# Kernel tuning notes

Hardware: AMD Instinct MI355X
Metric: run time of the kernel (lower is better)

Reference implementation:

```python
import jax, jax.numpy as jnp
import numpy as np

B, T, D, N, K, H = 2, 2048, 3584, 16, 8, 256
WINDOW = 1024
SOFT_CAP = 50.0
SCALAR = 0.0625  # head_dim ** -0.5
BASE = 10000.0
K_MASK = -2.3819763e38


def apply_rope(x, pos):
    # x: [B, S, heads, H], pos: [B, S]
    frac = 2.0 * jnp.arange(H // 2, dtype=jnp.float32) / H
    timescale = BASE ** frac  # [H/2]
    sinusoid = pos[..., None].astype(jnp.float32) / timescale  # [B, S, H/2]
    sinusoid = sinusoid[..., None, :]  # [B, S, 1, H/2]
    sin, cos = jnp.sin(sinusoid), jnp.cos(sinusoid)
    first, second = jnp.split(x, 2, axis=-1)
    out = jnp.concatenate([first * cos - second * sin,
                           second * cos + first * sin], axis=-1)
    return out.astype(x.dtype)


def setup_inputs() -> dict:
    key = jax.random.key(0)
    ks = jax.random.split(key, 4)
    x = jax.random.normal(ks[0], (B, T, D), jnp.float32)
    q_w = jax.random.normal(ks[1], (N, D, H), jnp.float32) * 0.02
    kv_w = jax.random.normal(ks[2], (2, K, D, H), jnp.float32) * 0.02
    o_w = jax.random.normal(ks[3], (N, H, D), jnp.float32) * 0.02
    segment_pos = jnp.broadcast_to(jnp.arange(T, dtype=jnp.int32), (B, T))
    attn_mask = jnp.tril(jnp.ones((1, T, T), dtype=bool))  # causal [#B, T, S]
    return {"x": x, "segment_pos": segment_pos, "attn_mask": attn_mask,
            "q_w": q_w, "kv_w": kv_w, "o_w": o_w}


def reference(x, segment_pos, attn_mask, q_w, kv_w, o_w):
    # Projections (GQA path: num_kv_heads != num_heads)
    q = jnp.einsum('BTD,NDH->BTNH', x, q_w)
    kv = jnp.einsum('BSD,CKDH->CBSKH', x, kv_w)
    k, v = kv[0], kv[1]
    # RoPE on keys and queries, then query scaling
    k = apply_rope(k, segment_pos)
    q = apply_rope(q, segment_pos) * SCALAR
    # GQA: group N query heads over K kv heads
    G = N // K
    qg = q.reshape(B, T, K, G, H)
    logits = jnp.einsum('BTKGH,BSKH->BTKGS', qg, k).reshape(B, T, N, T)
    # Logit soft cap
    logits = jnp.tanh(logits / SOFT_CAP) * SOFT_CAP
    # Sliding-window causal mask (attn_mask is causal, S > window)
    mask = jnp.triu(attn_mask, 1 - WINDOW)  # [#B, T, S]
    padded = jnp.where(mask[:, :, None, :], logits, K_MASK)
    probs = jax.nn.softmax(padded, axis=-1).astype(k.dtype)
    enc = jnp.einsum('BTKGS,BSKH->BTKGH', probs.reshape(B, T, K, G, T), v)
    enc = enc.reshape(B, T, N, H)
    out = jnp.einsum('BTNH,NHD->BTD', enc, o_w)
    no_attended = jnp.all(mask == 0, axis=-1, keepdims=True)  # [#B, T, 1]
    return jnp.where(no_attended, jnp.zeros_like(out), out)
```

## Files before the change

kernel.cpp:

```cpp
#include <hip/hip_runtime.h>
#include <stdint.h>


typedef short bf16x8 __attribute__((ext_vector_type(8)));
typedef float f32x4 __attribute__((ext_vector_type(4)));

#define MFMA16(a, b, c) __builtin_amdgcn_mfma_f32_16x16x32_bf16((a), (b), (c), 0, 0, 0)

__device__ __forceinline__ uint16_t f2bf(float f) {
  uint32_t u = __builtin_bit_cast(uint32_t, f);
  u += 0x7FFFu + ((u >> 16) & 1u);
  return (uint16_t)(u >> 16);
}
__device__ __forceinline__ float bf2f(uint16_t u) {
  return __builtin_bit_cast(float, (uint32_t)u << 16);
}
__device__ __forceinline__ void async16(void* lds, const void* g) {
  __builtin_amdgcn_global_load_lds(
      (const __attribute__((address_space(1))) uint32_t*)g,
      (__attribute__((address_space(3))) uint32_t*)lds, 16, 0, 0);
}

__global__ void convert_x(const float* __restrict__ x, uint16_t* __restrict__ xb) {
  size_t i = ((size_t)blockIdx.x * 256 + threadIdx.x) * 8;
  f32x4 a = *(const f32x4*)(x + i);
  f32x4 b = *(const f32x4*)(x + i + 4);
  bf16x8 r;
  r[0] = (short)f2bf(a[0]); r[1] = (short)f2bf(a[1]);
  r[2] = (short)f2bf(a[2]); r[3] = (short)f2bf(a[3]);
  r[4] = (short)f2bf(b[0]); r[5] = (short)f2bf(b[1]);
  r[6] = (short)f2bf(b[2]); r[7] = (short)f2bf(b[3]);
  *(bf16x8*)(xb + i) = r;
}

__global__ void transpose_qkvw(const float* __restrict__ qw,
                               const float* __restrict__ kvw,
                               uint16_t* __restrict__ WqkvT) {
  __shared__ uint16_t tile[64][65];
  const int j0 = blockIdx.x * 64;
  const int d0 = blockIdx.y * 64;
  const int t = threadIdx.x;
  const int jl = t & 63;
  const int q4 = t >> 6;
  const int j = j0 + jl;
  const float* src;
  if (j0 < 4096) {
    src = qw + (size_t)(j >> 8) * 3584 * 256 + (j & 255);
  } else {
    int j2 = j - 4096;
    src = kvw + ((size_t)((j2 >> 11) * 8 + ((j2 >> 8) & 7)) * 3584) * 256 + (j2 & 255);
  }
#pragma unroll
  for (int r = 0; r < 16; ++r) {
    int dl = r * 4 + q4;
    tile[jl][dl] = f2bf(src[(size_t)(d0 + dl) * 256]);
  }
  __syncthreads();
#pragma unroll
  for (int r = 0; r < 16; ++r) {
    int jl2 = r * 4 + q4;
    WqkvT[(size_t)(j0 + jl2) * 3584 + d0 + jl] = tile[jl2][jl];
  }
}

__global__ void transpose_ow(const float* __restrict__ ow, uint16_t* __restrict__ WoT) {
  __shared__ uint16_t tile[64][65];
  const int d0 = blockIdx.x * 64;
  const int j0 = blockIdx.y * 64;
  const int t = threadIdx.x;
  const int c = t & 63;
  const int q4 = t >> 6;
#pragma unroll
  for (int r = 0; r < 16; ++r) {
    int jl = r * 4 + q4;
    tile[c][jl] = f2bf(ow[(size_t)(j0 + jl) * 3584 + d0 + c]);
  }
  __syncthreads();
#pragma unroll
  for (int r = 0; r < 16; ++r) {
    int dl = r * 4 + q4;
    WoT[(size_t)(d0 + dl) * 4096 + j0 + c] = tile[dl][c];
  }
}

template <int EPI>
__global__ __launch_bounds__(512, 2) void gemm256(
    const uint16_t* __restrict__ A, const uint16_t* __restrict__ Bt,
    int Kd, int Nc, int nbx,
    void* __restrict__ Oqv, uint16_t* __restrict__ Ok, uint16_t* __restrict__ Ov) {
  __shared__ uint16_t lds[4 * 16384];

  const int tid = threadIdx.x;
  const int lane = tid & 63;
  const int quad = lane >> 4;
  const int l15 = lane & 15;
  const int wave = tid >> 6;
  const int wm = wave & 1;
  const int wn = wave >> 1;

  const int nwg = gridDim.x;
  const int chunk = nwg >> 3;
  const int wg = blockIdx.x;
  const int swz = (wg & 7) * chunk + (wg >> 3);
  const int by = swz / nbx;
  const int bx = swz - by * nbx;
  const int m0 = by * 256;
  const int n0 = bx * 256;

  f32x4 acc[8][4];
#pragma unroll
  for (int i = 0; i < 8; ++i)
#pragma unroll
    for (int j = 0; j < 4; ++j) acc[i][j] = f32x4{0.f, 0.f, 0.f, 0.f};

  const int srow = tid >> 2;
  const int sck = tid & 3;
  const int gck0 = sck ^ ((srow >> 1) & 3);
  const int gck1 = sck ^ (((srow + 128) >> 1) & 3);
  const uint16_t* gA0 = A + (size_t)(m0 + srow) * Kd + gck0 * 8;
  const uint16_t* gA1 = A + (size_t)(m0 + srow + 128) * Kd + gck1 * 8;
  const uint16_t* gB0 = Bt + (size_t)(n0 + srow) * Kd + gck0 * 8;
  const uint16_t* gB1 = Bt + (size_t)(n0 + srow + 128) * Kd + gck1 * 8;

  const int T = Kd >> 5;

#pragma unroll
  for (int pt = 0; pt < 3; ++pt) {
    uint16_t* sd = lds + pt * 16384;
    const int kt = pt * 32;
    async16(sd + tid * 8, gA0 + kt);
    async16(sd + 4096 + tid * 8, gA1 + kt);
    async16(sd + 8192 + tid * 8, gB0 + kt);
    async16(sd + 12288 + tid * 8, gB1 + kt);
  }

  const int arow = wm * 128;
  const int brow = wn * 64;

  for (int t = 0; t < T; ++t) {
    const uint16_t* sA = lds + (t & 3) * 16384;
    const uint16_t* sB = sA + 8192;
    uint16_t* sd = lds + ((t + 3) & 3) * 16384;
    int ts = t + 3;
    if (ts >= T) ts = T - 1;
    const int ktS = ts * 32;

    asm volatile("s_waitcnt vmcnt(8)" ::: "memory");
    __builtin_amdgcn_s_barrier();
    __builtin_amdgcn_sched_barrier(0);

    async16(sd + tid * 8, gA0 + ktS);
    async16(sd + 4096 + tid * 8, gA1 + ktS);
    async16(sd + 8192 + tid * 8, gB0 + ktS);
    async16(sd + 12288 + tid * 8, gB1 + ktS);

    bf16x8 bfr[4], af[8];
#pragma unroll
    for (int fn = 0; fn < 4; ++fn) {
      const int r = brow + fn * 16 + l15;
      bfr[fn] = *(const bf16x8*)(sB + r * 32 + ((quad ^ ((r >> 1) & 3)) << 3));
    }
#pragma unroll
    for (int i = 0; i < 8; ++i) {
      const int r = arow + i * 16 + l15;
      af[i] = *(const bf16x8*)(sA + r * 32 + ((quad ^ ((r >> 1) & 3)) << 3));
    }
    __builtin_amdgcn_s_setprio(1);
#pragma unroll
    for (int i = 0; i < 8; ++i)
#pragma unroll
      for (int fn = 0; fn < 4; ++fn)
        acc[i][fn] = MFMA16(af[i], bfr[fn], acc[i][fn]);
    __builtin_amdgcn_s_setprio(0);
  }

  asm volatile("s_waitcnt vmcnt(0)" ::: "memory");

  const int rowb = m0 + wm * 128;
  const int colb = n0 + wn * 64;
  if (EPI == 0) {
    if (n0 < 4096) {
      uint16_t* Oq = (uint16_t*)Oqv;
#pragma unroll
      for (int fm = 0; fm < 8; ++fm)
#pragma unroll
        for (int fn = 0; fn < 4; ++fn) {
          const int r0 = rowb + fm * 16 + quad * 4;
          const int c = colb + fn * 16 + l15;
#pragma unroll
          for (int reg = 0; reg < 4; ++reg)
            Oq[(size_t)(r0 + reg) * 4096 + c] = f2bf(acc[fm][fn][reg]);
        }
    } else if (n0 < 6144) {
#pragma unroll
      for (int fm = 0; fm < 8; ++fm)
#pragma unroll
        for (int fn = 0; fn < 4; ++fn) {
          const int r0 = rowb + fm * 16 + quad * 4;
          const int c = colb + fn * 16 + l15 - 4096;
#pragma unroll
          for (int reg = 0; reg < 4; ++reg)
            Ok[(size_t)(r0 + reg) * 2048 + c] = f2bf(acc[fm][fn][reg]);
        }
    } else {
#pragma unroll
      for (int fm = 0; fm < 8; ++fm)
#pragma unroll
        for (int fn = 0; fn < 4; ++fn) {
          const int r0 = rowb + fm * 16 + quad * 4;
          const int c2 = colb + fn * 16 + l15 - 6144;
          const int kvh = c2 >> 8, h = c2 & 255;
          const int bb = r0 >> 11, tt = r0 & 2047;
          ushort4 pk;
          pk.x = f2bf(acc[fm][fn][0]);
          pk.y = f2bf(acc[fm][fn][1]);
          pk.z = f2bf(acc[fm][fn][2]);
          pk.w = f2bf(acc[fm][fn][3]);
          *(ushort4*)(Ov + ((((size_t)bb * 8 + kvh) * 256 + h) * 2048 + tt)) = pk;
        }
    }
  } else {
    float* Oq = (float*)Oqv;
#pragma unroll
    for (int fm = 0; fm < 8; ++fm)
#pragma unroll
      for (int fn = 0; fn < 4; ++fn) {
        const int r0 = rowb + fm * 16 + quad * 4;
        const int c = colb + fn * 16 + l15;
#pragma unroll
        for (int reg = 0; reg < 4; ++reg)
          Oq[(size_t)(r0 + reg) * Nc + c] = acc[fm][fn][reg];
      }
  }
}

__global__ void rope_kernel(uint16_t* __restrict__ Qb, uint16_t* __restrict__ Kb,
                            const int* __restrict__ segpos) {
  const size_t QN = (size_t)2 * 2048 * 16 * 128;
  size_t idx = (size_t)blockIdx.x * 256 + threadIdx.x;
  uint16_t* buf;
  size_t base;
  int i, t, b;
  bool isQ = idx < QN;
  if (isQ) {
    i = (int)(idx & 127);
    int nn = (int)((idx >> 7) & 15);
    t = (int)((idx >> 11) & 2047);
    b = (int)(idx >> 22);
    base = ((size_t)((b * 2048 + t) * 16 + nn) << 8) + i;
    buf = Qb;
  } else {
    size_t x2 = idx - QN;
    i = (int)(x2 & 127);
    int kh = (int)((x2 >> 7) & 7);
    t = (int)((x2 >> 10) & 2047);
    b = (int)(x2 >> 21);
    base = ((size_t)((b * 2048 + t) * 8 + kh) << 8) + i;
    buf = Kb;
  }
  float pos = (float)segpos[b * 2048 + t];
  float inv = exp2f((float)i * (-13.287712379549449f / 128.f));
  float ang = pos * inv;
  float sn = sinf(ang), cs = cosf(ang);
  float x1 = bf2f(buf[base]);
  float x2v = bf2f(buf[base + 128]);
  float o1 = x1 * cs - x2v * sn;
  float o2 = x2v * cs + x1 * sn;
  if (isQ) { o1 *= 0.0625f; o2 *= 0.0625f; }
  buf[base] = f2bf(o1);
  buf[base + 128] = f2bf(o2);
}

__global__ __launch_bounds__(512, 2) void attn_kernel(
    const uint16_t* __restrict__ Qb, const uint16_t* __restrict__ Kb,
    const uint16_t* __restrict__ Vt, uint16_t* __restrict__ enc) {
  __shared__ uint16_t Ks[2][64 * 256];
  __shared__ uint16_t Vs[2][256 * 64];
  __shared__ uint16_t Ps[8 * 16 * 72];
  const int tid = threadIdx.x;
  const int lane = tid & 63;
  const int wave = tid >> 6;
  const int quad = lane >> 4;
  const int l15 = lane & 15;

  const int bid = blockIdx.x;
  const int swz = (bid & 7) * 64 + (bid >> 3);
  const int qt0 = (swz & 31) * 64;
  const int y = swz >> 5;
  const int b = y >> 3;
  const int kvh = y & 7;
  const int g = wave & 1;
  const int wr = (wave >> 1) * 16;
  const int n = kvh * 2 + g;

  f32x4 oacc[16];
#pragma unroll
  for (int ht = 0; ht < 16; ++ht) oacc[ht] = f32x4{0.f, 0.f, 0.f, 0.f};
  float mrow[4], lrow[4];
#pragma unroll
  for (int r = 0; r < 4; ++r) { mrow[r] = -50.f; lrow[r] = 0.f; }

  const uint16_t* qptr =
      Qb + ((size_t)((b * 2048 + qt0 + wr + l15) * 16 + n) << 8) + quad * 8;
  bf16x8 q[8];
#pragma unroll
  for (int c = 0; c < 8; ++c) q[c] = *(const bf16x8*)(qptr + c * 32);

  const int krw = tid >> 5;
  const uint16_t* kg0 = Kb + (size_t)b * 4194304 + kvh * 256 +
                        (size_t)krw * 2048 + (((tid & 31) ^ krw) << 3);
  const int vrw = tid >> 3;
  const uint16_t* vg0 = Vt + ((size_t)(b * 8 + kvh) << 19) +
                        (size_t)vrw * 2048 + (((tid & 7) ^ (vrw & 7)) << 3);

  int lo = qt0 - 1023;
  if (lo < 0) lo = 0;
  const int s0_start = (lo >> 6) << 6;

#pragma unroll
  for (int r = 0; r < 4; ++r)
    async16(&Ks[0][r * 4096 + tid * 8], kg0 + (size_t)(s0_start + r * 16) * 2048);
#pragma unroll
  for (int r = 0; r < 4; ++r)
    async16(&Vs[0][r * 4096 + tid * 8], vg0 + (size_t)r * 131072 + s0_start);
  __syncthreads();

  int cur = 0;
  for (int s0 = s0_start; s0 <= qt0; s0 += 64, cur ^= 1) {
    if (s0 + 64 <= qt0) {
      uint16_t* kd = Ks[cur ^ 1];
      uint16_t* vd = Vs[cur ^ 1];
#pragma unroll
      for (int r = 0; r < 4; ++r)
        async16(kd + r * 4096 + tid * 8, kg0 + (size_t)(s0 + 64 + r * 16) * 2048);
#pragma unroll
      for (int r = 0; r < 4; ++r)
        async16(vd + r * 4096 + tid * 8, vg0 + (size_t)r * 131072 + (s0 + 64));
    }
    const uint16_t* ksb = Ks[cur];
    const uint16_t* vsb = Vs[cur];

    f32x4 sac[4];
#pragma unroll
    for (int j = 0; j < 4; ++j) sac[j] = f32x4{0.f, 0.f, 0.f, 0.f};
    __builtin_amdgcn_s_setprio(1);
#pragma unroll
    for (int c = 0; c < 8; ++c) {
#pragma unroll
      for (int j = 0; j < 4; ++j) {
        bf16x8 kf = *(const bf16x8*)(ksb + (j * 16 + l15) * 256 +
                                     (((c * 4 + quad) ^ l15) << 3));
        sac[j] = MFMA16(q[c], kf, sac[j]);
      }
    }
    __builtin_amdgcn_s_setprio(0);

#pragma unroll
    for (int reg = 0; reg < 4; ++reg) {
      const int t = qt0 + wr + quad * 4 + reg;
      float pv[4];
      float mx = -1e30f;
#pragma unroll
      for (int j = 0; j < 4; ++j) {
        int s = s0 + j * 16 + l15;
        float v = sac[j][reg];
        float e = __expf(v * 0.04f);
        float scv = 50.f - 100.f / (e + 1.f);
        bool valid = (s <= t) && (s + 1024 > t);
        v = valid ? scv : -1e30f;
        pv[j] = v;
        mx = fmaxf(mx, v);
      }
      mx = fmaxf(mx, __shfl_xor(mx, 1));
      mx = fmaxf(mx, __shfl_xor(mx, 2));
      mx = fmaxf(mx, __shfl_xor(mx, 4));
      mx = fmaxf(mx, __shfl_xor(mx, 8));
      float mold = mrow[reg];
      if (!__all(mx <= mold + 8.f)) {
        float mnew = fmaxf(mold, mx);
        float alpha = __expf(mold - mnew);
        lrow[reg] *= alpha;
#pragma unroll
        for (int ht = 0; ht < 16; ++ht) oacc[ht][reg] *= alpha;
        mrow[reg] = mnew;
        mold = mnew;
      }
      float rs = 0.f;
#pragma unroll
      for (int j = 0; j < 4; ++j) {
        float p = __expf(pv[j] - mold);
        pv[j] = p;
        rs += p;
      }
      rs += __shfl_xor(rs, 1);
      rs += __shfl_xor(rs, 2);
      rs += __shfl_xor(rs, 4);
      rs += __shfl_xor(rs, 8);
      lrow[reg] += rs;
      const int r = quad * 4 + reg;
#pragma unroll
      for (int j = 0; j < 4; ++j)
        Ps[wave * 1152 + r * 72 + j * 16 + l15] = f2bf(pv[j]);
    }

#pragma unroll
    for (int c2 = 0; c2 < 2; ++c2) {
      const int lch = c2 * 4 + quad;
      bf16x8 pf = *(const bf16x8*)(Ps + wave * 1152 + l15 * 72 + lch * 8);
      __builtin_amdgcn_s_setprio(1);
#pragma unroll
      for (int ht = 0; ht < 16; ++ht) {
        bf16x8 vf = *(const bf16x8*)(vsb + (ht * 16 + l15) * 64 +
                                     ((lch ^ (l15 & 7)) << 3));
        oacc[ht] = MFMA16(pf, vf, oacc[ht]);
      }
      __builtin_amdgcn_s_setprio(0);
    }
    __syncthreads();
  }

#pragma unroll
  for (int reg = 0; reg < 4; ++reg) {
    float li = 1.f / lrow[reg];
    const int t = qt0 + wr + quad * 4 + reg;
    size_t base = ((size_t)((b * 2048 + t) * 16 + n) << 8) + l15;
#pragma unroll
    for (int ht = 0; ht < 16; ++ht)
      enc[base + ht * 16] = f2bf(oacc[ht][reg] * li);
  }
}

extern "C" void kernel_launch(void* const* d_in, const int* in_sizes, int n_in,
                              void* d_out, int out_size, void* d_ws, size_t ws_size,
                              hipStream_t stream) {
  const float* x = (const float*)d_in[0];
  const int* segpos = (const int*)d_in[1];
  const float* qw = (const float*)d_in[3];
  const float* kvw = (const float*)d_in[4];
  const float* ow = (const float*)d_in[5];
  float* out = (float*)d_out;

  uint16_t* ws = (uint16_t*)d_ws;
  uint16_t* WqkvT = ws;
  uint16_t* enc = ws;
  uint16_t* xb = ws + (size_t)29360128;
  uint16_t* WoT = ws + (size_t)29360128;
  uint16_t* Qb = ws + (size_t)44040192;
  uint16_t* Kb = ws + (size_t)60817408;
  uint16_t* Vt = ws + (size_t)69206016;

  convert_x<<<7168, 256, 0, stream>>>(x, xb);
  transpose_qkvw<<<dim3(128, 56), 256, 0, stream>>>(qw, kvw, WqkvT);
  gemm256<0><<<dim3(512), dim3(512), 0, stream>>>(xb, WqkvT, 3584, 8192, 32, Qb, Kb, Vt);
  rope_kernel<<<49152, 256, 0, stream>>>(Qb, Kb, segpos);
  attn_kernel<<<dim3(512), dim3(512), 0, stream>>>(Qb, Kb, Vt, enc);
  transpose_ow<<<dim3(56, 64), 256, 0, stream>>>(ow, WoT);
  gemm256<1><<<dim3(224), dim3(512), 0, stream>>>(enc, WoT, 4096, 3584, 14, out, nullptr, nullptr);
}
```

Measured before the change: 737.8 us.

## Restructure GEMM mainloop to BK=64 double-buffered half-tile staging with interleaved loads

The 256x256 GEMM mainloop moves from a 4-stage ring of K=32 tiles to two K=64 buffers. Each buffer holds A and B split into 128-row halves, with an XOR swizzle over 8 chunks. Each K step is split into four phases that each load part of the A fragments, issue one async half-tile stage for the next or next-but-one step, and run 16 MFMAs between barriers. The aim is to interleave global-to-LDS traffic with compute at finer grain and halve the outer loop count, at the cost of more barriers per K step.

```diff
diff --git a/kernel.cpp b/kernel.cpp
--- a/kernel.cpp
+++ b/kernel.cpp
@@ -88,7 +88,7 @@
     const uint16_t* __restrict__ A, const uint16_t* __restrict__ Bt,
     int Kd, int Nc, int nbx,
     void* __restrict__ Oqv, uint16_t* __restrict__ Ok, uint16_t* __restrict__ Ov) {
-  __shared__ uint16_t lds[4 * 16384];
+  __shared__ uint16_t lds[2 * 32768];
 
   const int tid = threadIdx.x;
   const int lane = tid & 63;
@@ -113,65 +113,88 @@
 #pragma unroll
     for (int j = 0; j < 4; ++j) acc[i][j] = f32x4{0.f, 0.f, 0.f, 0.f};
 
-  const int srow = tid >> 2;
-  const int sck = tid & 3;
-  const int gck0 = sck ^ ((srow >> 1) & 3);
-  const int gck1 = sck ^ (((srow + 128) >> 1) & 3);
-  const uint16_t* gA0 = A + (size_t)(m0 + srow) * Kd + gck0 * 8;
-  const uint16_t* gA1 = A + (size_t)(m0 + srow + 128) * Kd + gck1 * 8;
-  const uint16_t* gB0 = Bt + (size_t)(n0 + srow) * Kd + gck0 * 8;
-  const uint16_t* gB1 = Bt + (size_t)(n0 + srow + 128) * Kd + gck1 * 8;
-
-  const int T = Kd >> 5;
-
-#pragma unroll
-  for (int pt = 0; pt < 3; ++pt) {
-    uint16_t* sd = lds + pt * 16384;
-    const int kt = pt * 32;
-    async16(sd + tid * 8, gA0 + kt);
-    async16(sd + 4096 + tid * 8, gA1 + kt);
-    async16(sd + 8192 + tid * 8, gB0 + kt);
-    async16(sd + 12288 + tid * 8, gB1 + kt);
-  }
-
-  const int arow = wm * 128;
-  const int brow = wn * 64;
-
-  for (int t = 0; t < T; ++t) {
-    const uint16_t* sA = lds + (t & 3) * 16384;
-    const uint16_t* sB = sA + 8192;
-    uint16_t* sd = lds + ((t + 3) & 3) * 16384;
-    int ts = t + 3;
-    if (ts >= T) ts = T - 1;
-    const int ktS = ts * 32;
-
-    asm volatile("s_waitcnt vmcnt(8)" ::: "memory");
-    __builtin_amdgcn_s_barrier();
-    __builtin_amdgcn_sched_barrier(0);
-
-    async16(sd + tid * 8, gA0 + ktS);
-    async16(sd + 4096 + tid * 8, gA1 + ktS);
-    async16(sd + 8192 + tid * 8, gB0 + ktS);
-    async16(sd + 12288 + tid * 8, gB1 + ktS);
-
-    bf16x8 bfr[4], af[8];
-#pragma unroll
-    for (int fn = 0; fn < 4; ++fn) {
-      const int r = brow + fn * 16 + l15;
-      bfr[fn] = *(const bf16x8*)(sB + r * 32 + ((quad ^ ((r >> 1) & 3)) << 3));
-    }
-#pragma unroll
-    for (int i = 0; i < 8; ++i) {
-      const int r = arow + i * 16 + l15;
-      af[i] = *(const bf16x8*)(sA + r * 32 + ((quad ^ ((r >> 1) & 3)) << 3));
-    }
-    __builtin_amdgcn_s_setprio(1);
-#pragma unroll
-    for (int i = 0; i < 8; ++i)
-#pragma unroll
-      for (int fn = 0; fn < 4; ++fn)
-        acc[i][fn] = MFMA16(af[i], bfr[fn], acc[i][fn]);
-    __builtin_amdgcn_s_setprio(0);
+  const int srow = tid >> 3;
+  const int scol = (((tid & 7) ^ (srow & 7)) << 3);
+  const uint16_t* gA = A + (size_t)m0 * Kd;
+  const uint16_t* gB = Bt + (size_t)n0 * Kd;
+
+  auto stageA = [&](int b, int h, int m) {
+    uint16_t* d = lds + b * 32768 + h * 8192;
+    const uint16_t* s = gA + (size_t)(h * 128 + srow) * Kd + m * 64 + scol;
+    async16(d + tid * 8, s);
+    async16(d + 4096 + tid * 8, s + (size_t)64 * Kd);
+  };
+  auto stageB = [&](int b, int h, int m) {
+    uint16_t* d = lds + b * 32768 + 16384 + h * 8192;
+    const uint16_t* s = gB + (size_t)(h * 128 + srow) * Kd + m * 64 + scol;
+    async16(d + tid * 8, s);
+    async16(d + 4096 + tid * 8, s + (size_t)64 * Kd);
+  };
+
+  const int NK = Kd >> 6;
+
+  stageB(0, 0, 0); stageB(0, 1, 0);
+  stageA(0, 0, 0); stageA(0, 1, 0);
+  stageB(1, 0, 1); stageB(1, 1, 1);
+  asm volatile("s_waitcnt vmcnt(4)" ::: "memory");
+  __builtin_amdgcn_s_barrier();
+
+  const int amh = wm;
+  const int bmh = wn >> 1;
+  const int browl = (wn & 1) * 64;
+
+  for (int j = 0; j < NK; ++j) {
+    const uint16_t* bufr = lds + (j & 1) * 32768;
+    const uint16_t* sAh = bufr + amh * 8192;
+    const uint16_t* sBh = bufr + 16384 + bmh * 8192;
+    const int jp1 = (j + 1 < NK) ? j + 1 : NK - 1;
+    const int jp2 = (j + 2 < NK) ? j + 2 : NK - 1;
+    const int bA = (j + 1) & 1;
+    const int bB = j & 1;
+
+    bf16x8 bfr[4][2];
+#pragma unroll
+    for (int q = 0; q < 4; ++q) {
+      if (q == 0) {
+#pragma unroll
+        for (int bn = 0; bn < 4; ++bn)
+#pragma unroll
+          for (int s = 0; s < 2; ++s) {
+            const int r = browl + bn * 16 + l15;
+            bfr[bn][s] = *(const bf16x8*)(
+                sBh + r * 64 + (((s * 4 + quad) ^ (r & 7)) << 3));
+          }
+      }
+      bf16x8 af[2][2];
+#pragma unroll
+      for (int i = 0; i < 2; ++i)
+#pragma unroll
+        for (int s = 0; s < 2; ++s) {
+          const int r = (2 * q + i) * 16 + l15;
+          af[i][s] = *(const bf16x8*)(
+              sAh + r * 64 + (((s * 4 + quad) ^ (r & 7)) << 3));
+        }
+      if (q == 0) stageA(bA, 0, jp1);
+      else if (q == 1) stageA(bA, 1, jp1);
+      else if (q == 2) stageB(bB, 0, jp2);
+      else {
+        stageB(bB, 1, jp2);
+        asm volatile("s_waitcnt vmcnt(4)" ::: "memory");
+      }
+      __builtin_amdgcn_s_barrier();
+      asm volatile("s_waitcnt lgkmcnt(0)" ::: "memory");
+      __builtin_amdgcn_sched_barrier(0);
+      __builtin_amdgcn_s_setprio(1);
+#pragma unroll
+      for (int i = 0; i < 2; ++i)
+#pragma unroll
+        for (int n = 0; n < 4; ++n)
+#pragma unroll
+          for (int s = 0; s < 2; ++s)
+            acc[2 * q + i][n] = MFMA16(af[i][s], bfr[n][s], acc[2 * q + i][n]);
+      __builtin_amdgcn_s_setprio(0);
+      __builtin_amdgcn_s_barrier();
+    }
   }
 
   asm volatile("s_waitcnt vmcnt(0)" ::: "memory");
```

After: 762.8 us. 1.03x slower.
